# Kernel tuning notes

Hardware: AMD Instinct MI355X
Metric: run time of the kernel (lower is better)

## Reference

```python
import jax, jax.numpy as jnp
import numpy as np

B, S, HID, NH, HD, INTER, NB = 4, 4096, 2048, 32, 64, 8192, 8
EPS = 1e-5
MEM_EPS = 1e-6


def rmsnorm(x, w, eps=EPS):
    return x * jax.lax.rsqrt(jnp.mean(x * x, axis=-1, keepdims=True) + eps) * w


def hbit_linear(x, w):
    # BitNet b1.58: ternary weights (absmean scale) + int8 per-token activation quant (STE).
    ws = jnp.mean(jnp.abs(w)) + 1e-8
    wq = jnp.round(jnp.clip(w / ws, -1.0, 1.0)) * ws
    w_eff = w + jax.lax.stop_gradient(wq - w)
    xs = 127.0 / jnp.clip(jnp.max(jnp.abs(x), axis=-1, keepdims=True), 1e-5, None)
    xq = jnp.clip(jnp.round(x * xs), -128.0, 127.0) / xs
    x_eff = x + jax.lax.stop_gradient(xq - x)
    return x_eff @ w_eff.T


def infini_attention(xn, wq, wk, wv, wo, beta):
    # xn: [B,S,HID]; segment-wise causal local attention + compressive linear memory.
    def proj(w):
        return (xn @ w.T).reshape(B, S, NH, HD).transpose(0, 2, 1, 3)  # [B,H,S,D]

    q, k, v = proj(wq), proj(wk), proj(wv)
    seg = S // NB

    def to_segs(t):
        return t.reshape(B, NH, NB, seg, HD).transpose(2, 0, 1, 3, 4)  # [NB,B,H,seg,D]

    qs, ks, vs = to_segs(q), to_segs(k), to_segs(v)
    mask = jnp.tril(jnp.ones((seg, seg), bool))
    g = jax.nn.sigmoid(beta)[None, :, None, None]  # per-head memory/local mix
    scale = 1.0 / np.sqrt(HD)

    def step(carry, inp):
        M, z = carry  # M:[B,H,D,D], z:[B,H,D]
        qc, kc, vc = inp
        sq = jax.nn.elu(qc) + 1.0
        sk = jax.nn.elu(kc) + 1.0
        a_mem = jnp.einsum('bhsd,bhde->bhse', sq, M) / (
            jnp.einsum('bhsd,bhd->bhs', sq, z)[..., None] + MEM_EPS)
        scores = jnp.einsum('bhqd,bhkd->bhqk', qc, kc) * scale
        scores = jnp.where(mask, scores, -1e9)
        a_loc = jnp.einsum('bhqk,bhkd->bhqd', jax.nn.softmax(scores, axis=-1), vc)
        M = M + jnp.einsum('bhsd,bhse->bhde', sk, vc)
        z = z + sk.sum(axis=2)
        out = g * a_mem + (1.0 - g) * a_loc
        return (M, z), out

    M0 = jnp.zeros((B, NH, HD, HD), xn.dtype)
    z0 = jnp.zeros((B, NH, HD), xn.dtype)
    _, outs = jax.lax.scan(step, (M0, z0), (qs, ks, vs))  # [NB,B,H,seg,D]
    out = outs.transpose(1, 2, 0, 3, 4).reshape(B, NH, S, HD)
    out = out.transpose(0, 2, 1, 3).reshape(B, S, HID)
    return out @ wo.T


def setup_inputs() -> dict:
    key = jax.random.key(0)
    ks = jax.random.split(key, 12)
    std = 0.02
    return {
        'x': jax.random.normal(ks[0], (B, S, HID), jnp.float32),
        'wq': jax.random.normal(ks[1], (HID, HID), jnp.float32) * std,
        'wk': jax.random.normal(ks[2], (HID, HID), jnp.float32) * std,
        'wv': jax.random.normal(ks[3], (HID, HID), jnp.float32) * std,
        'wo': jax.random.normal(ks[4], (HID, HID), jnp.float32) * std,
        'beta': jnp.zeros((NH,), jnp.float32),
        'gate': jnp.zeros((1,), jnp.float32),
        'attn_norm_w': jnp.ones((HID,), jnp.float32),
        'mlp_norm_w': jnp.ones((HID,), jnp.float32),
        'attn_res_norm_w': jnp.ones((HID,), jnp.float32),
        'attn_res_scale': jnp.full((1,), 0.1, jnp.float32),
        'mlp_res_norm_w': jnp.ones((HID,), jnp.float32),
        'mlp_res_scale': jnp.full((1,), 0.1, jnp.float32),
        'ffn_up_w': jax.random.normal(ks[5], (2 * INTER, HID), jnp.float32) * std,
        'ffn_down_w': jax.random.normal(ks[6], (HID, INTER), jnp.float32) * std,
    }


def reference(x, wq, wk, wv, wo, beta, gate, attn_norm_w, mlp_norm_w,
              attn_res_norm_w, attn_res_scale, mlp_res_norm_w, mlp_res_scale,
              ffn_up_w, ffn_down_w):
    residual = x
    xn = rmsnorm(x, attn_norm_w)
    infini_out = infini_attention(xn, wq, wk, wv, wo, beta)
    gated = jax.nn.sigmoid(gate) * infini_out
    x = residual + attn_res_scale * rmsnorm(gated, attn_res_norm_w)
    residual = x
    xn = rmsnorm(x, mlp_norm_w)
    up = hbit_linear(xn, ffn_up_w)
    gate_up, value = jnp.split(up, 2, axis=-1)
    mlp_out = hbit_linear(jax.nn.silu(gate_up) * value, ffn_down_w)
    x = residual + mlp_res_scale * rmsnorm(mlp_out, mlp_res_norm_w)
    return x
```

## Files before the change

kernel.cpp:

```cpp
#include <hip/hip_runtime.h>
#include <cstdint>
#include <cstddef>

typedef unsigned int u32;
typedef unsigned short u16;
typedef __bf16 bf16x8 __attribute__((ext_vector_type(8)));
typedef float f32x4 __attribute__((ext_vector_type(4)));
typedef float f32x16 __attribute__((ext_vector_type(16)));
typedef int i32x4 __attribute__((ext_vector_type(4)));

#define DEV static __device__ __forceinline__

DEV float bf2f(u16 u) { u32 x = ((u32)u) << 16; return __builtin_bit_cast(float, x); }
DEV u16 f2bf(float f) {
  u32 u = __builtin_bit_cast(u32, f);
  u32 r = (u + 0x7fffu + ((u >> 16) & 1u)) >> 16;
  return (u16)r;
}
DEV u32 pkbf(float a, float b) {
  __bf16 ba = (__bf16)a, bb = (__bf16)b;
  return (u32)__builtin_bit_cast(u16, ba) | ((u32)__builtin_bit_cast(u16, bb) << 16);
}
DEV u32 pk4i8(float a, float b, float c, float d) {
  return (u32)(unsigned char)(char)a | ((u32)(unsigned char)(char)b << 8) |
         ((u32)(unsigned char)(char)c << 16) | ((u32)(unsigned char)(char)d << 24);
}
DEV void bf8tof(const uint4 v, float* f) {
  f[0] = bf2f((u16)(v.x & 0xffffu)); f[1] = bf2f((u16)(v.x >> 16));
  f[2] = bf2f((u16)(v.y & 0xffffu)); f[3] = bf2f((u16)(v.y >> 16));
  f[4] = bf2f((u16)(v.z & 0xffffu)); f[5] = bf2f((u16)(v.z >> 16));
  f[6] = bf2f((u16)(v.w & 0xffffu)); f[7] = bf2f((u16)(v.w >> 16));
}
DEV uint4 f8tobf(const float* f) {
  uint4 r;
  r.x = (u32)f2bf(f[0]) | ((u32)f2bf(f[1]) << 16);
  r.y = (u32)f2bf(f[2]) | ((u32)f2bf(f[3]) << 16);
  r.z = (u32)f2bf(f[4]) | ((u32)f2bf(f[5]) << 16);
  r.w = (u32)f2bf(f[6]) | ((u32)f2bf(f[7]) << 16);
  return r;
}
DEV float sigmoidf_(float x) { return 1.f / (1.f + expf(-x)); }

DEV float wred_sum(float v) {
  #pragma unroll
  for (int m = 32; m; m >>= 1) v += __shfl_xor(v, m, 64);
  return v;
}
DEV float wred_max(float v) {
  #pragma unroll
  for (int m = 32; m; m >>= 1) v = fmaxf(v, __shfl_xor(v, m, 64));
  return v;
}
DEV float block_sum(float v, float* red, int nw) {
  v = wred_sum(v);
  int w = threadIdx.x >> 6, l = threadIdx.x & 63;
  if (l == 0) red[w] = v;
  __syncthreads();
  float t = red[0];
  for (int i = 1; i < nw; ++i) t += red[i];
  __syncthreads();
  return t;
}
DEV float block_max(float v, float* red, int nw) {
  v = wred_max(v);
  int w = threadIdx.x >> 6, l = threadIdx.x & 63;
  if (l == 0) red[w] = v;
  __syncthreads();
  float t = red[0];
  for (int i = 1; i < nw; ++i) t = fmaxf(t, red[i]);
  __syncthreads();
  return t;
}
DEV void gload16(const void* g, void* l) {
  __builtin_amdgcn_global_load_lds((const __attribute__((address_space(1))) void*)g,
                                   (__attribute__((address_space(3))) void*)l, 16, 0, 0);
}
DEV bf16x8 ldfrag(const u16* p) {
  uint4 u = *(const uint4*)p;
  return __builtin_bit_cast(bf16x8, u);
}

#define BN_ 4
#define S_ 4096
#define HID_ 2048
#define NH_ 32
#define HD_ 64
#define INTER_ 8192
#define NBSEG_ 8
#define SEG_ 512
#define TOK_ 16384
#define CHROWS_ 4096
#define LDQ_ 6144

__global__ __launch_bounds__(256) void castf2b(const float* __restrict__ a, u16* __restrict__ o) {
  size_t idx = ((size_t)blockIdx.x * 256 + threadIdx.x) * 4;
  float4 v = *(const float4*)(a + idx);
  float f[4] = {v.x, v.y, v.z, v.w};
  uint2 r;
  r.x = (u32)f2bf(f[0]) | ((u32)f2bf(f[1]) << 16);
  r.y = (u32)f2bf(f[2]) | ((u32)f2bf(f[3]) << 16);
  *(uint2*)(o + idx) = r;
}

__global__ __launch_bounds__(256) void absmean_part(const float* __restrict__ w, float* __restrict__ part) {
  __shared__ float red[4];
  size_t base = (size_t)blockIdx.x * 16384 + threadIdx.x * 4;
  float s = 0.f;
  #pragma unroll
  for (int i = 0; i < 16; ++i) {
    float4 v = *(const float4*)(w + base + (size_t)i * 1024);
    s += fabsf(v.x) + fabsf(v.y) + fabsf(v.z) + fabsf(v.w);
  }
  float t = block_sum(s, red, 4);
  if (threadIdx.x == 0) part[blockIdx.x] = t;
}

__global__ __launch_bounds__(256) void absmean_fin(const float* __restrict__ part, int n, float invN, float* __restrict__ outp) {
  __shared__ float red[4];
  float s = 0.f;
  for (int i = threadIdx.x; i < n; i += 256) s += part[i];
  float t = block_sum(s, red, 4);
  if (threadIdx.x == 0) outp[0] = t * invN + 1e-8f;
}

__global__ __launch_bounds__(256) void ternarize_i8(const float* __restrict__ w, const float* __restrict__ wsp, char* __restrict__ o) {
  size_t idx = ((size_t)blockIdx.x * 256 + threadIdx.x) * 4;
  const float inv = 1.f / wsp[0];
  float4 v = *(const float4*)(w + idx);
  float q0 = rintf(fminf(fmaxf(v.x * inv, -1.f), 1.f));
  float q1 = rintf(fminf(fmaxf(v.y * inv, -1.f), 1.f));
  float q2 = rintf(fminf(fmaxf(v.z * inv, -1.f), 1.f));
  float q3 = rintf(fminf(fmaxf(v.w * inv, -1.f), 1.f));
  *(u32*)(o + idx) = pk4i8(q0, q1, q2, q3);
}

__global__ __launch_bounds__(256) void rmsnorm_cast(const float* __restrict__ x, const float* __restrict__ wn, u16* __restrict__ o) {
  __shared__ float red[4];
  const int r = blockIdx.x, tid = threadIdx.x;
  const float* xr = x + (size_t)r * HID_;
  float vx[8];
  #pragma unroll
  for (int i = 0; i < 2; ++i) {
    float4 t = *(const float4*)(xr + tid * 8 + i * 4);
    vx[i * 4 + 0] = t.x; vx[i * 4 + 1] = t.y; vx[i * 4 + 2] = t.z; vx[i * 4 + 3] = t.w;
  }
  float ss = 0.f;
  #pragma unroll
  for (int j = 0; j < 8; ++j) ss += vx[j] * vx[j];
  float tot = block_sum(ss, red, 4);
  float rstd = rsqrtf(tot * (1.f / HID_) + 1e-5f);
  float wv[8];
  #pragma unroll
  for (int i = 0; i < 2; ++i) {
    float4 t = *(const float4*)(wn + tid * 8 + i * 4);
    wv[i * 4 + 0] = t.x; wv[i * 4 + 1] = t.y; wv[i * 4 + 2] = t.z; wv[i * 4 + 3] = t.w;
  }
  float ov[8];
  #pragma unroll
  for (int j = 0; j < 8; ++j) ov[j] = vx[j] * rstd * wv[j];
  *(uint4*)(o + (size_t)r * HID_ + tid * 8) = f8tobf(ov);
}

__global__ __launch_bounds__(256) void resid1_rms2(const float* __restrict__ x, const u16* __restrict__ ao,
    const float* __restrict__ gatep, const float* __restrict__ w1, const float* __restrict__ rsp,
    const float* __restrict__ w2, float* __restrict__ x2, char* __restrict__ xq, float* __restrict__ xs1) {
  __shared__ float red[4];
  const int r = blockIdx.x, tid = threadIdx.x;
  const float g = sigmoidf_(gatep[0]);
  const float rs = rsp[0];
  uint4 av = *(const uint4*)(ao + (size_t)r * HID_ + tid * 8);
  float f[8]; bf8tof(av, f);
  float ss = 0.f;
  #pragma unroll
  for (int j = 0; j < 8; ++j) { f[j] *= g; ss += f[j] * f[j]; }
  float tot = block_sum(ss, red, 4);
  float rstd1 = rsqrtf(tot * (1.f / HID_) + 1e-5f);
  const float* xr = x + (size_t)r * HID_;
  float xv2[8];
  #pragma unroll
  for (int i = 0; i < 2; ++i) {
    float4 xv = *(const float4*)(xr + tid * 8 + i * 4);
    float4 wv = *(const float4*)(w1 + tid * 8 + i * 4);
    xv2[i * 4 + 0] = xv.x + rs * f[i * 4 + 0] * rstd1 * wv.x;
    xv2[i * 4 + 1] = xv.y + rs * f[i * 4 + 1] * rstd1 * wv.y;
    xv2[i * 4 + 2] = xv.z + rs * f[i * 4 + 2] * rstd1 * wv.z;
    xv2[i * 4 + 3] = xv.w + rs * f[i * 4 + 3] * rstd1 * wv.w;
  }
  float* o = x2 + (size_t)r * HID_;
  *(float4*)(o + tid * 8) = float4{xv2[0], xv2[1], xv2[2], xv2[3]};
  *(float4*)(o + tid * 8 + 4) = float4{xv2[4], xv2[5], xv2[6], xv2[7]};
  float ss2 = 0.f;
  #pragma unroll
  for (int j = 0; j < 8; ++j) ss2 += xv2[j] * xv2[j];
  float tot2 = block_sum(ss2, red, 4);
  float rstd2 = rsqrtf(tot2 * (1.f / HID_) + 1e-5f);
  float xn[8]; float mx = 0.f;
  #pragma unroll
  for (int i = 0; i < 2; ++i) {
    float4 wv = *(const float4*)(w2 + tid * 8 + i * 4);
    xn[i * 4 + 0] = xv2[i * 4 + 0] * rstd2 * wv.x;
    xn[i * 4 + 1] = xv2[i * 4 + 1] * rstd2 * wv.y;
    xn[i * 4 + 2] = xv2[i * 4 + 2] * rstd2 * wv.z;
    xn[i * 4 + 3] = xv2[i * 4 + 3] * rstd2 * wv.w;
  }
  #pragma unroll
  for (int j = 0; j < 8; ++j) mx = fmaxf(mx, fabsf(xn[j]));
  float bm = block_max(mx, red, 4);
  float xs = 127.f / fmaxf(bm, 1e-5f);
  float q[8];
  #pragma unroll
  for (int j = 0; j < 8; ++j) q[j] = fminf(fmaxf(rintf(xn[j] * xs), -128.f), 127.f);
  uint2 pw;
  pw.x = pk4i8(q[0], q[1], q[2], q[3]);
  pw.y = pk4i8(q[4], q[5], q[6], q[7]);
  *(uint2*)(xq + (size_t)r * HID_ + tid * 8) = pw;
  if (tid == 0) xs1[r] = xs;
}

__global__ __launch_bounds__(256) void quant_h_i8(const u16* __restrict__ hb, char* __restrict__ hq, float* __restrict__ xs2) {
  __shared__ float red[4];
  const int r = blockIdx.x, tid = threadIdx.x;
  const u16* hr = hb + (size_t)r * INTER_ + tid * 32;
  float f[32];
  #pragma unroll
  for (int k = 0; k < 4; ++k) {
    uint4 v = *(const uint4*)(hr + k * 8);
    bf8tof(v, &f[k * 8]);
  }
  float mx = 0.f;
  #pragma unroll
  for (int j = 0; j < 32; ++j) mx = fmaxf(mx, fabsf(f[j]));
  float bm = block_max(mx, red, 4);
  float xs = 127.f / fmaxf(bm, 1e-5f);
  u32 pw[8];
  #pragma unroll
  for (int k = 0; k < 8; ++k) {
    float q[4];
    #pragma unroll
    for (int j = 0; j < 4; ++j) q[j] = fminf(fmaxf(rintf(f[k * 4 + j] * xs), -128.f), 127.f);
    pw[k] = pk4i8(q[0], q[1], q[2], q[3]);
  }
  char* oq = hq + (size_t)r * INTER_ + tid * 32;
  *(uint4*)oq = uint4{pw[0], pw[1], pw[2], pw[3]};
  *(uint4*)(oq + 16) = uint4{pw[4], pw[5], pw[6], pw[7]};
  if (tid == 0) xs2[r] = xs;
}

__global__ __launch_bounds__(256) void final_resid(const float* __restrict__ x2, const u16* __restrict__ mlp,
    const float* __restrict__ wn, const float* __restrict__ rsp, float* __restrict__ out) {
  __shared__ float red[4];
  const int r = blockIdx.x, tid = threadIdx.x;
  const float rs = rsp[0];
  uint4 mv = *(const uint4*)(mlp + (size_t)r * HID_ + tid * 8);
  float f[8]; bf8tof(mv, f);
  float ss = 0.f;
  #pragma unroll
  for (int j = 0; j < 8; ++j) ss += f[j] * f[j];
  float tot = block_sum(ss, red, 4);
  float rstd = rsqrtf(tot * (1.f / HID_) + 1e-5f);
  const float* xr = x2 + (size_t)r * HID_;
  float* o = out + (size_t)r * HID_;
  #pragma unroll
  for (int i = 0; i < 2; ++i) {
    float4 xv = *(const float4*)(xr + tid * 8 + i * 4);
    float4 wv = *(const float4*)(wn + tid * 8 + i * 4);
    float4 ov;
    ov.x = xv.x + rs * f[i * 4 + 0] * rstd * wv.x;
    ov.y = xv.y + rs * f[i * 4 + 1] * rstd * wv.y;
    ov.z = xv.z + rs * f[i * 4 + 2] * rstd * wv.z;
    ov.w = xv.w + rs * f[i * 4 + 3] * rstd * wv.w;
    *(float4*)(o + tid * 8 + i * 4) = ov;
  }
}

template<int NBN>
__global__ __launch_bounds__(512, 2)
void gemm_bt2(const u16* __restrict__ A, const u16* __restrict__ Bw, u16* __restrict__ C,
              int K, int ldc) {
  __shared__ __align__(16) u16 As[128 * 64];
  __shared__ __align__(16) u16 Bs[256 * 64];
  const int tid = threadIdx.x;
  const int w = tid >> 6, lane = tid & 63;
  const int l15 = lane & 15, l4 = lane >> 4;
  const int wr = (w >> 2) * 64, wc = (w & 3) * 64;
  int id = blockIdx.x;
  const int cpx = (int)gridDim.x >> 3;
  id = (id & 7) * cpx + (id >> 3);
  const int bm = id / NBN, bn = id % NBN;
  const u16* Ag = A + (size_t)bm * 128 * K;
  const u16* Bg = Bw + (size_t)bn * 256 * K;
  f32x4 acc[4][4] = {};
  for (int kk = 0; kk < K; kk += 64) {
    #pragma unroll
    for (int p = 0; p < 2; ++p) {
      const int idx = tid + p * 512;
      const int row = idx >> 3, slot = idx & 7;
      const int ss = slot ^ (row & 7);
      gload16(Ag + (size_t)row * K + kk + ss * 8, &As[idx * 8]);
    }
    #pragma unroll
    for (int p = 0; p < 4; ++p) {
      const int idx = tid + p * 512;
      const int row = idx >> 3, slot = idx & 7;
      const int ss = slot ^ (row & 7);
      gload16(Bg + (size_t)row * K + kk + ss * 8, &Bs[idx * 8]);
    }
    __syncthreads();
    bf16x8 af[4][2], bb[4][2];
    #pragma unroll
    for (int i = 0; i < 4; ++i) {
      const int ra = wr + i * 16 + l15;
      const int rb = wc + i * 16 + l15;
      #pragma unroll
      for (int k2 = 0; k2 < 2; ++k2) {
        const int g8 = k2 * 4 + l4;
        af[i][k2] = ldfrag(&As[ra * 64 + ((g8 ^ (ra & 7)) * 8)]);
        bb[i][k2] = ldfrag(&Bs[rb * 64 + ((g8 ^ (rb & 7)) * 8)]);
      }
    }
    #pragma unroll
    for (int i = 0; i < 4; ++i)
      #pragma unroll
      for (int j = 0; j < 4; ++j)
        #pragma unroll
        for (int k2 = 0; k2 < 2; ++k2)
          acc[i][j] = __builtin_amdgcn_mfma_f32_16x16x32_bf16(af[i][k2], bb[j][k2], acc[i][j], 0, 0, 0);
    __syncthreads();
  }
  #pragma unroll
  for (int i = 0; i < 4; ++i) {
    #pragma unroll
    for (int r = 0; r < 4; ++r) {
      const int row = bm * 128 + wr + i * 16 + l4 * 4 + r;
      #pragma unroll
      for (int j = 0; j < 4; ++j) {
        const int col = bn * 256 + wc + j * 16 + l15;
        C[(size_t)row * ldc + col] = f2bf(acc[i][j][r]);
      }
    }
  }
}

__global__ __launch_bounds__(512, 2)
void gemm_up_i8(const char* __restrict__ A, const char* __restrict__ Bw, u16* __restrict__ H,
                const float* __restrict__ wsp, const float* __restrict__ xs) {
  const int K = HID_;
  __shared__ __align__(16) char As[128 * 128];
  __shared__ __align__(16) char Gs[128 * 128];
  __shared__ __align__(16) char Vs[128 * 128];
  const int tid = threadIdx.x;
  const int w = tid >> 6, lane = tid & 63;
  const int l15 = lane & 15, l4 = lane >> 4;
  const int wr = (w >> 2) * 64, wc = (w & 3) * 32;
  int id = blockIdx.x;
  const int cpx = (int)gridDim.x >> 3;
  id = (id & 7) * cpx + (id >> 3);
  const int bm = id & 31, bn = id >> 5;
  const char* Ag = A + (size_t)bm * 128 * K;
  const char* Gg = Bw + (size_t)bn * 128 * K;
  const char* Vg = Bw + ((size_t)INTER_ + bn * 128) * K;
  i32x4 ag[4][2] = {}, av[4][2] = {};
  for (int kk = 0; kk < K; kk += 128) {
    #pragma unroll
    for (int p = 0; p < 2; ++p) {
      const int idx = tid + p * 512;
      const int row = idx >> 3, slot = idx & 7;
      const int ss = slot ^ (row & 7);
      gload16(Ag + (size_t)row * K + kk + ss * 16, &As[idx * 16]);
      gload16(Gg + (size_t)row * K + kk + ss * 16, &Gs[idx * 16]);
      gload16(Vg + (size_t)row * K + kk + ss * 16, &Vs[idx * 16]);
    }
    __syncthreads();
    i32x4 af_[4][2], gf_[2][2], vf_[2][2];
    #pragma unroll
    for (int i = 0; i < 4; ++i) {
      const int r = wr + i * 16 + l15;
      #pragma unroll
      for (int k2 = 0; k2 < 2; ++k2) {
        const int j = k2 * 4 + l4;
        af_[i][k2] = *(const i32x4*)&As[r * 128 + ((j ^ (r & 7)) * 16)];
      }
    }
    #pragma unroll
    for (int jj = 0; jj < 2; ++jj) {
      const int r = wc + jj * 16 + l15;
      #pragma unroll
      for (int k2 = 0; k2 < 2; ++k2) {
        const int j = k2 * 4 + l4;
        gf_[jj][k2] = *(const i32x4*)&Gs[r * 128 + ((j ^ (r & 7)) * 16)];
        vf_[jj][k2] = *(const i32x4*)&Vs[r * 128 + ((j ^ (r & 7)) * 16)];
      }
    }
    #pragma unroll
    for (int i = 0; i < 4; ++i)
      #pragma unroll
      for (int jj = 0; jj < 2; ++jj)
        #pragma unroll
        for (int k2 = 0; k2 < 2; ++k2) {
          ag[i][jj] = __builtin_amdgcn_mfma_i32_16x16x64_i8(af_[i][k2], gf_[jj][k2], ag[i][jj], 0, 0, 0);
          av[i][jj] = __builtin_amdgcn_mfma_i32_16x16x64_i8(af_[i][k2], vf_[jj][k2], av[i][jj], 0, 0, 0);
        }
    __syncthreads();
  }
  const float ws0 = wsp[0];
  #pragma unroll
  for (int i = 0; i < 4; ++i) {
    #pragma unroll
    for (int r = 0; r < 4; ++r) {
      const int row = bm * 128 + wr + i * 16 + l4 * 4 + r;
      const float scl = ws0 / xs[row];
      #pragma unroll
      for (int jj = 0; jj < 2; ++jj) {
        const int col = bn * 128 + wc + jj * 16 + l15;
        const float og = (float)ag[i][jj][r] * scl;
        const float ov = (float)av[i][jj][r] * scl;
        const float hv = og * ov / (1.f + expf(-og));
        H[(size_t)row * INTER_ + col] = f2bf(hv);
      }
    }
  }
}

__global__ __launch_bounds__(256, 2)
void gemm_dn_i8(const char* __restrict__ A, const char* __restrict__ Bw, u16* __restrict__ C,
                const float* __restrict__ wsp, const float* __restrict__ xs) {
  const int N = HID_, K = INTER_;
  __shared__ __align__(16) char As[128 * 128];
  __shared__ __align__(16) char Bs[128 * 128];
  const int tid = threadIdx.x;
  const int wv = tid >> 6, lane = tid & 63;
  const int l15 = lane & 15, l4 = lane >> 4;
  const int wr = (wv >> 1) * 64, wc = (wv & 1) * 64;
  const int bm = blockIdx.y, bn = blockIdx.x;
  const char* Ag = A + (size_t)bm * 128 * K;
  const char* Bg = Bw + (size_t)bn * 128 * K;
  i32x4 acc[4][4] = {};
  for (int kk = 0; kk < K; kk += 128) {
    #pragma unroll
    for (int p = 0; p < 4; ++p) {
      const int idx = tid + p * 256;
      const int row = idx >> 3, slot = idx & 7;
      const int ss = slot ^ (row & 7);
      gload16(Ag + (size_t)row * K + kk + ss * 16, &As[idx * 16]);
      gload16(Bg + (size_t)row * K + kk + ss * 16, &Bs[idx * 16]);
    }
    __syncthreads();
    i32x4 af_[4][2], bb_[4][2];
    #pragma unroll
    for (int i = 0; i < 4; ++i) {
      const int ra = wr + i * 16 + l15;
      const int rb = wc + i * 16 + l15;
      #pragma unroll
      for (int k2 = 0; k2 < 2; ++k2) {
        const int j = k2 * 4 + l4;
        af_[i][k2] = *(const i32x4*)&As[ra * 128 + ((j ^ (ra & 7)) * 16)];
        bb_[i][k2] = *(const i32x4*)&Bs[rb * 128 + ((j ^ (rb & 7)) * 16)];
      }
    }
    #pragma unroll
    for (int i = 0; i < 4; ++i)
      #pragma unroll
      for (int j = 0; j < 4; ++j)
        #pragma unroll
        for (int k2 = 0; k2 < 2; ++k2)
          acc[i][j] = __builtin_amdgcn_mfma_i32_16x16x64_i8(af_[i][k2], bb_[j][k2], acc[i][j], 0, 0, 0);
    __syncthreads();
  }
  const float ws0 = wsp[0];
  #pragma unroll
  for (int i = 0; i < 4; ++i) {
    #pragma unroll
    for (int r = 0; r < 4; ++r) {
      const int row = bm * 128 + wr + i * 16 + l4 * 4 + r;
      const float scl = ws0 / xs[row];
      #pragma unroll
      for (int j = 0; j < 4; ++j) {
        const int col = bn * 128 + wc + j * 16 + l15;
        C[(size_t)row * N + col] = f2bf((float)acc[i][j][r] * scl);
      }
    }
  }
}

DEV void write_otile(const f32x16 oc, float invl, char* stgB, u16* alocrow,
                     int da, int l31, int hi, int lane) {
  #pragma unroll
  for (int r = 0; r < 16; ++r) {
    const int dl = (r & 3) + 8 * (r >> 2) + 4 * hi;
    *(u16*)(stgB + l31 * 64 + ((dl * 2) ^ ((l31 & 3) << 4))) = f2bf(oc[r] * invl);
  }
  #pragma unroll
  for (int p = 0; p < 2; ++p) {
    const int s = lane >> 1;
    const int d8 = (lane & 1) * 8 + p * 16;
    const uint4 val = *(const uint4*)(stgB + s * 64 + ((d8 * 2) ^ ((s & 3) << 4)));
    *(uint4*)(alocrow + (size_t)s * HD_ + da * 32 + d8) = val;
  }
}

__global__ __launch_bounds__(512)
void attn_local_mfma(const u16* __restrict__ q, const u16* __restrict__ k, const u16* __restrict__ v,
                     u16* __restrict__ aloc, float* __restrict__ Useg, float* __restrict__ yseg, int ldq) {
  __shared__ __align__(16) u16 Ks[512 * 64];
  __shared__ __align__(16) u16 VT[64 * 512];
  __shared__ __align__(16) u16 SP[9216];
  const int bid = blockIdx.x;
  const int c = bid >> 7, bh = bid & 127;
  const int b = bh >> 5, h = bh & 31;
  const int tid = threadIdx.x, w = tid >> 6, lane = tid & 63;
  const int l31 = lane & 31, hi = lane >> 5;
  const size_t rowbase = ((size_t)b * S_ + c * SEG_) * (size_t)ldq + h * HD_;
  const u16* qg = q + rowbase;
  const u16* kg = k + rowbase;
  const u16* vg = v + rowbase;
  char* KsB = (char*)Ks;
  char* VTB = (char*)VT;
  #pragma unroll
  for (int p = 0; p < 8; ++p) {
    const int idx = tid + p * 512;
    const int t = idx >> 3, dg = idx & 7;
    const uint4 kv = *(const uint4*)(kg + (size_t)t * ldq + dg * 8);
    *(uint4*)(KsB + t * 128 + ((dg * 16) ^ ((t & 7) << 4))) = kv;
  }
  {
    const int t = w * 64 + lane;
    #pragma unroll
    for (int dg = 0; dg < 8; ++dg) {
      const uint4 vv = *(const uint4*)(vg + (size_t)t * ldq + dg * 8);
      const u16* e = (const u16*)&vv;
      #pragma unroll
      for (int j = 0; j < 8; ++j) {
        const int d = dg * 8 + j;
        *(u16*)(VTB + d * 1024 + ((t * 2) ^ ((d & 7) << 4))) = e[j];
      }
    }
  }
  uint4 qf[2][4];
  #pragma unroll
  for (int qi = 0; qi < 2; ++qi) {
    const int qt = qi == 0 ? w : 15 - w;
    #pragma unroll
    for (int ks = 0; ks < 4; ++ks)
      qf[qi][ks] = *(const uint4*)(qg + (size_t)(qt * 32 + l31) * ldq + ks * 16 + hi * 8);
  }
  __syncthreads();

  const size_t arow = (size_t)(b * NH_ + h) * S_ + c * SEG_;
  const int swzk = (l31 & 7) << 4;
  char* stgB = (char*)SP + w * 2048;
  #pragma unroll
  for (int qi = 0; qi < 2; ++qi) {
    const int qt = qi == 0 ? w : 15 - w;
    f32x16 o0 = {}, o1 = {};
    float m = -3e38f, l = 0.f;
    const int nb = qt + 1;
    for (int tb = 0; tb < nb; ++tb) {
      f32x16 st = {};
      #pragma unroll
      for (int ks = 0; ks < 4; ++ks) {
        const uint4 ka = *(const uint4*)(KsB + (tb * 32 + l31) * 128 + (((ks * 16 + hi * 8) * 2) ^ swzk));
        st = __builtin_amdgcn_mfma_f32_32x32x16_bf16(__builtin_bit_cast(bf16x8, ka),
                                                     __builtin_bit_cast(bf16x8, qf[qi][ks]), st, 0, 0, 0);
      }
      if (tb == nb - 1) {
        #pragma unroll
        for (int r = 0; r < 16; ++r) {
          const int tl = (r & 3) + 8 * (r >> 2) + 4 * hi;
          if (tl > l31) st[r] = -3e38f;
        }
      }
      float tm = st[0];
      #pragma unroll
      for (int r = 1; r < 16; ++r) tm = fmaxf(tm, st[r]);
      tm = fmaxf(tm, __shfl_xor(tm, 32, 64));
      const float mn = fmaxf(m, tm);
      const float fac = __expf((m - mn) * 0.125f);
      float pr[16]; float ps = 0.f;
      #pragma unroll
      for (int r = 0; r < 16; ++r) { pr[r] = __expf((st[r] - mn) * 0.125f); ps += pr[r]; }
      ps += __shfl_xor(ps, 32, 64);
      l = l * fac + ps;
      m = mn;
      #pragma unroll
      for (int r = 0; r < 16; ++r) { o0[r] *= fac; o1[r] *= fac; }
      #pragma unroll
      for (int c2 = 0; c2 < 2; ++c2) {
        const int bi = c2 * 8;
        const u32 a0 = pkbf(pr[bi + 0], pr[bi + 1]);
        const u32 a1 = pkbf(pr[bi + 2], pr[bi + 3]);
        const u32 a2 = pkbf(pr[bi + 4], pr[bi + 5]);
        const u32 a3 = pkbf(pr[bi + 6], pr[bi + 7]);
        const u32 x0 = (u32)__shfl_xor((int)a0, 32, 64);
        const u32 x1 = (u32)__shfl_xor((int)a1, 32, 64);
        const u32 x2 = (u32)__shfl_xor((int)a2, 32, 64);
        const u32 x3 = (u32)__shfl_xor((int)a3, 32, 64);
        uint4 pw;
        pw.x = hi ? x2 : a0;
        pw.y = hi ? x3 : a1;
        pw.z = hi ? a2 : x0;
        pw.w = hi ? a3 : x1;
        const bf16x8 pfr = __builtin_bit_cast(bf16x8, pw);
        const int tO = (tb * 32 + c2 * 16 + hi * 8) * 2;
        const uint4 v0 = *(const uint4*)(VTB + l31 * 1024 + (tO ^ swzk));
        const uint4 v1 = *(const uint4*)(VTB + (32 + l31) * 1024 + (tO ^ swzk));
        o0 = __builtin_amdgcn_mfma_f32_32x32x16_bf16(__builtin_bit_cast(bf16x8, v0), pfr, o0, 0, 0, 0);
        o1 = __builtin_amdgcn_mfma_f32_32x32x16_bf16(__builtin_bit_cast(bf16x8, v1), pfr, o1, 0, 0, 0);
      }
    }
    const float invl = 1.f / l;
    u16* alocrow = aloc + (arow + qt * 32) * HD_;
    write_otile(o0, invl, stgB, alocrow, 0, l31, hi, lane);
    write_otile(o1, invl, stgB, alocrow, 1, l31, hi, lane);
  }

  __syncthreads();
  float* Ured = (float*)SP;
  float* yred = (float*)((char*)SP + 16384);
  for (int i = tid; i < 4096; i += 512) Ured[i] = 0.f;
  yred[tid] = 0.f;
  __syncthreads();
  f32x16 u00 = {}, u01 = {}, u10 = {}, u11 = {};
  float y0 = 0.f, y1 = 0.f;
  #pragma unroll
  for (int kc = 0; kc < 4; ++kc) {
    const int t0 = w * 64 + kc * 16 + hi * 8;
    uint4 af[2];
    #pragma unroll
    for (int da2 = 0; da2 < 2; ++da2) {
      const int d = da2 * 32 + l31;
      u32 wds[4];
      #pragma unroll
      for (int jp = 0; jp < 4; ++jp) {
        const int ta = t0 + jp * 2;
        const int tb2 = ta + 1;
        const float kfa = bf2f(*(const u16*)(KsB + ta * 128 + ((d * 2) ^ ((ta & 7) << 4))));
        const float kfb = bf2f(*(const u16*)(KsB + tb2 * 128 + ((d * 2) ^ ((tb2 & 7) << 4))));
        const float sa = kfa > 0.f ? kfa + 1.f : __expf(kfa);
        const float sb = kfb > 0.f ? kfb + 1.f : __expf(kfb);
        if (da2 == 0) y0 += sa + sb; else y1 += sa + sb;
        wds[jp] = pkbf(sa, sb);
      }
      af[da2].x = wds[0]; af[da2].y = wds[1]; af[da2].z = wds[2]; af[da2].w = wds[3];
    }
    const int tO = t0 * 2;
    const uint4 vb0 = *(const uint4*)(VTB + l31 * 1024 + (tO ^ swzk));
    const uint4 vb1 = *(const uint4*)(VTB + (32 + l31) * 1024 + (tO ^ swzk));
    const bf16x8 a0f = __builtin_bit_cast(bf16x8, af[0]);
    const bf16x8 a1f = __builtin_bit_cast(bf16x8, af[1]);
    const bf16x8 b0f = __builtin_bit_cast(bf16x8, vb0);
    const bf16x8 b1f = __builtin_bit_cast(bf16x8, vb1);
    u00 = __builtin_amdgcn_mfma_f32_32x32x16_bf16(a0f, b0f, u00, 0, 0, 0);
    u01 = __builtin_amdgcn_mfma_f32_32x32x16_bf16(a0f, b1f, u01, 0, 0, 0);
    u10 = __builtin_amdgcn_mfma_f32_32x32x16_bf16(a1f, b0f, u10, 0, 0, 0);
    u11 = __builtin_amdgcn_mfma_f32_32x32x16_bf16(a1f, b1f, u11, 0, 0, 0);
  }
  y0 += __shfl_xor(y0, 32, 64);
  y1 += __shfl_xor(y1, 32, 64);
  if (hi == 0) { yred[w * 64 + l31] = y0; yred[w * 64 + 32 + l31] = y1; }
  for (int ww = 0; ww < 8; ++ww) {
    if (w == ww) {
      #pragma unroll
      for (int r = 0; r < 16; ++r) {
        const int dl = (r & 3) + 8 * (r >> 2) + 4 * hi;
        Ured[dl * 64 + l31]            += u00[r];
        Ured[dl * 64 + 32 + l31]       += u01[r];
        Ured[(32 + dl) * 64 + l31]     += u10[r];
        Ured[(32 + dl) * 64 + 32 + l31]+= u11[r];
      }
    }
    __syncthreads();
  }
  float* Ug = Useg + (size_t)(c * 128 + bh) * 4096;
  for (int i = tid; i < 4096; i += 512) Ug[i] = Ured[i];
  if (tid < 64) {
    float a2 = 0.f;
    #pragma unroll
    for (int ww = 0; ww < 8; ++ww) a2 += yred[ww * 64 + tid];
    yseg[(size_t)(c * 128 + bh) * 64 + tid] = a2;
  }
}

__global__ __launch_bounds__(256)
void attn_prefix(const float* __restrict__ Useg, const float* __restrict__ yseg,
                 float* __restrict__ Mpre, float* __restrict__ zpre) {
  const int bh = blockIdx.x, tid = threadIdx.x;
  for (int idx = tid; idx < 4096; idx += 256) {
    float a2 = 0.f;
    #pragma unroll
    for (int c = 0; c < 8; ++c) {
      const size_t o = ((size_t)(c * 128 + bh)) * 4096 + idx;
      Mpre[o] = a2;
      a2 += Useg[o];
    }
  }
  if (tid < 64) {
    float a2 = 0.f;
    #pragma unroll
    for (int c = 0; c < 8; ++c) {
      const size_t o = ((size_t)(c * 128 + bh)) * 64 + tid;
      zpre[o] = a2;
      a2 += yseg[o];
    }
  }
}

__global__ __launch_bounds__(512)
void attn_combine(const u16* __restrict__ q, const u16* __restrict__ aloc,
                  const float* __restrict__ Mpre, const float* __restrict__ zpre,
                  const float* __restrict__ beta, u16* __restrict__ attno, int ldq) {
  __shared__ __align__(16) u16 MbT[64 * 64];
  __shared__ float z_lds[64];
  __shared__ float amem[8][16 * 65];
  const int bid = blockIdx.x;
  const int c = bid >> 7, bh = bid & 127;
  const int b = bh >> 5, h = bh & 31;
  const int tid = threadIdx.x, w = tid >> 6, lane = tid & 63;
  const int l15 = lane & 15, l4 = lane >> 4;
  const size_t pre = (size_t)(c * 128 + bh);
  char* MbB = (char*)MbT;
  for (int i = tid; i < 4096; i += 512) {
    const int d = i >> 6, e = i & 63;
    *(u16*)(MbB + (((e * 64 + d) * 2) ^ ((e & 7) << 4))) = f2bf(Mpre[pre * 4096 + i]);
  }
  if (tid < 64) z_lds[tid] = zpre[pre * 64 + tid];
  __syncthreads();
  bf16x8 bb[2][4];
  #pragma unroll
  for (int ks = 0; ks < 2; ++ks)
    #pragma unroll
    for (int jt = 0; jt < 4; ++jt) {
      const int e = jt * 16 + l15;
      const uint4 u = *(const uint4*)(MbB + (((e * 64 + ks * 32 + l4 * 8) * 2) ^ ((e & 7) << 4)));
      bb[ks][jt] = __builtin_bit_cast(bf16x8, u);
    }
  const float g = sigmoidf_(beta[h]);
  const float og = 1.f - g;
  const u16* qg = q + ((size_t)b * S_ + c * SEG_) * ldq + h * HD_;
  const size_t arow = (size_t)(b * NH_ + h) * S_ + c * SEG_;
  u16* orow = attno + ((size_t)b * S_ + c * SEG_) * HID_ + h * HD_;
  const int rr = lane >> 2, cq = (lane & 3) * 16;
  #pragma unroll
  for (int mi = 0; mi < 4; ++mi) {
    const int s0 = w * 64 + mi * 16;
    f32x4 acc[4] = {};
    float pd = 0.f;
    #pragma unroll
    for (int ks = 0; ks < 2; ++ks) {
      const uint4 qv = *(const uint4*)(qg + (size_t)(s0 + l15) * ldq + ks * 32 + l4 * 8);
      float f[8]; bf8tof(qv, f);
      float sq[8];
      #pragma unroll
      for (int j = 0; j < 8; ++j) {
        sq[j] = f[j] > 0.f ? f[j] + 1.f : __expf(f[j]);
        pd = fmaf(sq[j], z_lds[ks * 32 + l4 * 8 + j], pd);
      }
      uint4 pw;
      pw.x = pkbf(sq[0], sq[1]); pw.y = pkbf(sq[2], sq[3]);
      pw.z = pkbf(sq[4], sq[5]); pw.w = pkbf(sq[6], sq[7]);
      const bf16x8 af = __builtin_bit_cast(bf16x8, pw);
      #pragma unroll
      for (int jt = 0; jt < 4; ++jt)
        acc[jt] = __builtin_amdgcn_mfma_f32_16x16x32_bf16(af, bb[ks][jt], acc[jt], 0, 0, 0);
    }
    pd += __shfl_xor(pd, 16, 64);
    pd += __shfl_xor(pd, 32, 64);
    pd += 1e-6f;
    float dinv[4];
    #pragma unroll
    for (int r = 0; r < 4; ++r) dinv[r] = 1.f / __shfl(pd, l4 * 4 + r, 64);
    #pragma unroll
    for (int jt = 0; jt < 4; ++jt)
      #pragma unroll
      for (int r = 0; r < 4; ++r)
        amem[w][(l4 * 4 + r) * 65 + jt * 16 + l15] = acc[jt][r] * dinv[r];
    const int s = s0 + rr;
    const u16* alr = aloc + (arow + s) * HD_ + cq;
    const uint4 a0 = *(const uint4*)alr;
    const uint4 a1 = *(const uint4*)(alr + 8);
    float alf[16];
    bf8tof(a0, alf); bf8tof(a1, alf + 8);
    float ov[16];
    #pragma unroll
    for (int t = 0; t < 16; ++t)
      ov[t] = g * amem[w][rr * 65 + cq + t] + og * alf[t];
    *(uint4*)(orow + (size_t)s * HID_ + cq) = f8tobf(ov);
    *(uint4*)(orow + (size_t)s * HID_ + cq + 8) = f8tobf(ov + 8);
  }
}

extern "C" void kernel_launch(void* const* d_in, const int* in_sizes, int n_in,
                              void* d_out, int out_size, void* d_ws, size_t ws_size,
                              hipStream_t stream) {
  const float* x    = (const float*)d_in[0];
  const float* wq   = (const float*)d_in[1];
  const float* wk   = (const float*)d_in[2];
  const float* wv   = (const float*)d_in[3];
  const float* wo   = (const float*)d_in[4];
  const float* beta = (const float*)d_in[5];
  const float* gate = (const float*)d_in[6];
  const float* anw  = (const float*)d_in[7];
  const float* mnw  = (const float*)d_in[8];
  const float* arnw = (const float*)d_in[9];
  const float* arsc = (const float*)d_in[10];
  const float* mrnw = (const float*)d_in[11];
  const float* mrsc = (const float*)d_in[12];
  const float* fup  = (const float*)d_in[13];
  const float* fdn  = (const float*)d_in[14];

  char* W = (char*)d_ws;
  const size_t MB = 1ull << 20;
  u16*   xn1   = (u16*)(W + 0);
  u16*   attno = (u16*)(W + 0);
  u16*   mlpb  = (u16*)(W + 0);
  u16*   qkv   = (u16*)(W + 64 * MB);
  char*  xq1   = (char*)(W + 64 * MB);
  u16*   aob   = (u16*)(W + 128 * MB);
  u16*   hbuf  = (u16*)(W + 128 * MB);
  u16*   alocb = (u16*)(W + 256 * MB);
  float* x2    = (float*)(W + 192 * MB);
  float* Useg  = (float*)(W + 320 * MB);
  float* Mpre  = (float*)(W + 336 * MB);
  float* yseg  = (float*)(W + 352 * MB);
  float* zpre  = (float*)(W + 352 * MB + 262144);
  float* xs1   = (float*)(W + 352 * MB + 524288);
  float* xs2   = (float*)(W + 352 * MB + 589824);
  float* wsu   = (float*)(W + 352 * MB + 655360);
  float* wsd   = (float*)(W + 352 * MB + 655616);
  float* partU = (float*)(W + 352 * MB + 655872);
  float* partD = (float*)(W + 352 * MB + 664064);
  u16*   w16qkv= (u16*)(W + 353 * MB);
  u16*   w16o  = (u16*)(W + 377 * MB);
  char*  wqup  = (char*)(W + 385 * MB);
  char*  wqdn  = (char*)(W + 417 * MB);
  char*  hq    = (char*)(W + 433 * MB);

  castf2b<<<4096, 256, 0, stream>>>(wq, w16qkv);
  castf2b<<<4096, 256, 0, stream>>>(wk, w16qkv + (size_t)HID_ * HID_);
  castf2b<<<4096, 256, 0, stream>>>(wv, w16qkv + 2 * (size_t)HID_ * HID_);
  castf2b<<<4096, 256, 0, stream>>>(wo, w16o);
  absmean_part<<<2048, 256, 0, stream>>>(fup, partU);
  absmean_part<<<1024, 256, 0, stream>>>(fdn, partD);
  absmean_fin<<<1, 256, 0, stream>>>(partU, 2048, 1.f / 33554432.f, wsu);
  absmean_fin<<<1, 256, 0, stream>>>(partD, 1024, 1.f / 16777216.f, wsd);
  ternarize_i8<<<32768, 256, 0, stream>>>(fup, wsu, wqup);
  ternarize_i8<<<16384, 256, 0, stream>>>(fdn, wsd, wqdn);

  rmsnorm_cast<<<16384, 256, 0, stream>>>(x, anw, xn1);
  gemm_bt2<24><<<3072, 512, 0, stream>>>(xn1, w16qkv, qkv, HID_, LDQ_);
  attn_local_mfma<<<1024, 512, 0, stream>>>(qkv, qkv + HID_, qkv + 2 * HID_, alocb, Useg, yseg, LDQ_);
  attn_prefix<<<128, 256, 0, stream>>>(Useg, yseg, Mpre, zpre);
  attn_combine<<<1024, 512, 0, stream>>>(qkv, alocb, Mpre, zpre, beta, attno, LDQ_);
  gemm_bt2<8><<<1024, 512, 0, stream>>>(attno, w16o, aob, HID_, HID_);
  resid1_rms2<<<16384, 256, 0, stream>>>(x, aob, gate, arnw, arsc, mnw, x2, xq1, xs1);

  for (int cc = 0; cc < 4; ++cc) {
    const size_t base = (size_t)cc * CHROWS_;
    gemm_up_i8<<<2048, 512, 0, stream>>>(xq1 + base * HID_, wqup, hbuf, wsu, xs1 + base);
    quant_h_i8<<<4096, 256, 0, stream>>>(hbuf, hq, xs2 + base);
    gemm_dn_i8<<<dim3(16, 32), 256, 0, stream>>>(hq, wqdn, mlpb + base * HID_, wsd, xs2 + base);
  }
  final_resid<<<16384, 256, 0, stream>>>(x2, mlpb, mrnw, mrsc, (float*)d_out);
}
```

Measured before the change: 1.975 ms.

## Double-buffer bf16 GEMM LDS tiles and shrink N tile to 128

The bf16 QKV and output-projection GEMM now ping-pongs two LDS buffers, so the global loads for the next K slice are issued before the MFMAs on the current slice run. This removes one barrier per iteration. The N tile drops from 256 to 128, which halves the per-wave accumulators and raises the occupancy hint to 4 blocks per CU, and the grids are doubled to cover the same output. In exchange, the A tile is reused less and more blocks reload the same A rows.

```diff
diff --git a/kernel.cpp b/kernel.cpp
--- a/kernel.cpp
+++ b/kernel.cpp
@@ -274,58 +274,66 @@
 }
 
 template<int NBN>
-__global__ __launch_bounds__(512, 2)
+__global__ __launch_bounds__(512, 4)
 void gemm_bt2(const u16* __restrict__ A, const u16* __restrict__ Bw, u16* __restrict__ C,
               int K, int ldc) {
-  __shared__ __align__(16) u16 As[128 * 64];
-  __shared__ __align__(16) u16 Bs[256 * 64];
+  __shared__ __align__(16) u16 As[2][128 * 64];
+  __shared__ __align__(16) u16 Bs[2][128 * 64];
   const int tid = threadIdx.x;
   const int w = tid >> 6, lane = tid & 63;
   const int l15 = lane & 15, l4 = lane >> 4;
-  const int wr = (w >> 2) * 64, wc = (w & 3) * 64;
+  const int wr = (w >> 2) * 64, wc = (w & 3) * 32;
   int id = blockIdx.x;
   const int cpx = (int)gridDim.x >> 3;
   id = (id & 7) * cpx + (id >> 3);
   const int bm = id / NBN, bn = id % NBN;
   const u16* Ag = A + (size_t)bm * 128 * K;
-  const u16* Bg = Bw + (size_t)bn * 256 * K;
-  f32x4 acc[4][4] = {};
+  const u16* Bg = Bw + (size_t)bn * 128 * K;
+  const int r0 = tid >> 3, s0 = (tid & 7) ^ (r0 & 7);
+  const int r1 = (tid + 512) >> 3, s1 = ((tid + 512) & 7) ^ (r1 & 7);
+  f32x4 acc[4][2] = {};
+  gload16(Ag + (size_t)r0 * K + s0 * 8, &As[0][tid * 8]);
+  gload16(Ag + (size_t)r1 * K + s1 * 8, &As[0][(tid + 512) * 8]);
+  gload16(Bg + (size_t)r0 * K + s0 * 8, &Bs[0][tid * 8]);
+  gload16(Bg + (size_t)r1 * K + s1 * 8, &Bs[0][(tid + 512) * 8]);
+  __syncthreads();
+  int cur = 0;
   for (int kk = 0; kk < K; kk += 64) {
-    #pragma unroll
-    for (int p = 0; p < 2; ++p) {
-      const int idx = tid + p * 512;
-      const int row = idx >> 3, slot = idx & 7;
-      const int ss = slot ^ (row & 7);
-      gload16(Ag + (size_t)row * K + kk + ss * 8, &As[idx * 8]);
-    }
-    #pragma unroll
-    for (int p = 0; p < 4; ++p) {
-      const int idx = tid + p * 512;
-      const int row = idx >> 3, slot = idx & 7;
-      const int ss = slot ^ (row & 7);
-      gload16(Bg + (size_t)row * K + kk + ss * 8, &Bs[idx * 8]);
-    }
-    __syncthreads();
-    bf16x8 af[4][2], bb[4][2];
+    const int nxt = kk + 64;
+    if (nxt < K) {
+      gload16(Ag + (size_t)r0 * K + nxt + s0 * 8, &As[cur ^ 1][tid * 8]);
+      gload16(Ag + (size_t)r1 * K + nxt + s1 * 8, &As[cur ^ 1][(tid + 512) * 8]);
+      gload16(Bg + (size_t)r0 * K + nxt + s0 * 8, &Bs[cur ^ 1][tid * 8]);
+      gload16(Bg + (size_t)r1 * K + nxt + s1 * 8, &Bs[cur ^ 1][(tid + 512) * 8]);
+    }
+    bf16x8 af[4][2], bb[2][2];
     #pragma unroll
     for (int i = 0; i < 4; ++i) {
       const int ra = wr + i * 16 + l15;
-      const int rb = wc + i * 16 + l15;
       #pragma unroll
       for (int k2 = 0; k2 < 2; ++k2) {
         const int g8 = k2 * 4 + l4;
-        af[i][k2] = ldfrag(&As[ra * 64 + ((g8 ^ (ra & 7)) * 8)]);
-        bb[i][k2] = ldfrag(&Bs[rb * 64 + ((g8 ^ (rb & 7)) * 8)]);
+        af[i][k2] = ldfrag(&As[cur][ra * 64 + ((g8 ^ (ra & 7)) * 8)]);
+      }
+    }
+    #pragma unroll
+    for (int j = 0; j < 2; ++j) {
+      const int rb = wc + j * 16 + l15;
+      #pragma unroll
+      for (int k2 = 0; k2 < 2; ++k2) {
+        const int g8 = k2 * 4 + l4;
+        bb[j][k2] = ldfrag(&Bs[cur][rb * 64 + ((g8 ^ (rb & 7)) * 8)]);
       }
     }
     #pragma unroll
     for (int i = 0; i < 4; ++i)
       #pragma unroll
-      for (int j = 0; j < 4; ++j)
+      for (int j = 0; j < 2; ++j)
         #pragma unroll
         for (int k2 = 0; k2 < 2; ++k2)
           acc[i][j] = __builtin_amdgcn_mfma_f32_16x16x32_bf16(af[i][k2], bb[j][k2], acc[i][j], 0, 0, 0);
     __syncthreads();
+    cur ^= 1;
   }
   #pragma unroll
   for (int i = 0; i < 4; ++i) {
@@ -333,8 +341,8 @@
     for (int r = 0; r < 4; ++r) {
       const int row = bm * 128 + wr + i * 16 + l4 * 4 + r;
       #pragma unroll
-      for (int j = 0; j < 4; ++j) {
-        const int col = bn * 256 + wc + j * 16 + l15;
+      for (int j = 0; j < 2; ++j) {
+        const int col = bn * 128 + wc + j * 16 + l15;
         C[(size_t)row * ldc + col] = f2bf(acc[i][j][r]);
       }
     }
@@ -846,11 +854,11 @@
   ternarize_i8<<<16384, 256, 0, stream>>>(fdn, wsd, wqdn);
 
   rmsnorm_cast<<<16384, 256, 0, stream>>>(x, anw, xn1);
-  gemm_bt2<24><<<3072, 512, 0, stream>>>(xn1, w16qkv, qkv, HID_, LDQ_);
+  gemm_bt2<48><<<6144, 512, 0, stream>>>(xn1, w16qkv, qkv, HID_, LDQ_);
   attn_local_mfma<<<1024, 512, 0, stream>>>(qkv, qkv + HID_, qkv + 2 * HID_, alocb, Useg, yseg, LDQ_);
   attn_prefix<<<128, 256, 0, stream>>>(Useg, yseg, Mpre, zpre);
   attn_combine<<<1024, 512, 0, stream>>>(qkv, alocb, Mpre, zpre, beta, attno, LDQ_);
-  gemm_bt2<8><<<1024, 512, 0, stream>>>(attno, w16o, aob, HID_, HID_);
+  gemm_bt2<16><<<2048, 512, 0, stream>>>(attno, w16o, aob, HID_, HID_);
   resid1_rms2<<<16384, 256, 0, stream>>>(x, aob, gate, arnw, arsc, mnw, x2, xq1, xs1);
 
   for (int cc = 0; cc < 4; ++cc) {
```

After: 2.078 ms. +5.2%, slower.
